# Kernel optimization log

Hardware: AMD Instinct MI355X
Metric: run time of the kernel (lower is better)

The kernel has to match this reference:

```python
import jax, jax.numpy as jnp
import numpy as np

B, N, D, R, NUM_HEADS, S = 8, 512, 256, 6, 3, 1000


def setup_inputs() -> dict:
    key = jax.random.key(0)
    ks = jax.random.split(key, 12)
    init = lambda k, shape: jax.random.normal(k, shape, jnp.float32) * 0.02
    return {
        "symbol_ids": jax.random.randint(ks[0], (B, N), 0, S),
        "positions": jax.random.normal(ks[1], (B, N, 2), jnp.float32),
        "sym_table": init(ks[2], (S, D)),
        "layer_table": init(ks[3], (S, D)),      # layer-0 interpretation embedding
        "rel_W": init(ks[4], (R, D, D)),          # per-relation Linear weights (in,out)
        "rel_b": init(ks[5], (R, D)),
        "h1_W": init(ks[6], (NUM_HEADS, D, D)),   # interpretation head Linear1
        "h1_b": init(ks[7], (NUM_HEADS, D)),
        "h2_W": init(ks[8], (NUM_HEADS, D)),      # interpretation head Linear2 (D->1)
        "h2_b": init(ks[9], (NUM_HEADS,)),
        "out_W": init(ks[10], (D, D)),
        "out_b": init(ks[11], (D,)),
    }


def _relation_type(dx, dy):
    # Vectorized version of PositionalGrammar._get_relation_type (if/elif chain)
    return jnp.select(
        [dy > 0.5, dy < -0.5, dx < -0.5, dx > 0.5,
         (jnp.abs(dx) < 0.3) & (jnp.abs(dy) < 0.3)],
        [0, 1, 2, 3, 4], 5)


def _positional_grammar(symbols, positions, rel_W, rel_b):
    # transformed[b,j] = symbols[b,j] + sum_{i!=j} (symbols[b,i] @ W_r(i,j) + b_r(i,j))
    dx = positions[:, None, :, 0] - positions[:, :, None, 0]  # [b,i,j]
    dy = positions[:, None, :, 1] - positions[:, :, None, 1]
    rel = _relation_type(dx, dy)                               # [b,i,j] int
    n = symbols.shape[1]
    not_self = ~jnp.eye(n, dtype=bool)
    # one-hot relation mask, self-pairs excluded: [b,i,j,r]
    M = ((rel[..., None] == jnp.arange(R)) & not_self[None, :, :, None]).astype(symbols.dtype)
    T = jnp.einsum('bid,rde->brie', symbols, rel_W)            # per-relation transform of sources
    contrib = jnp.einsum('bijr,brie->bje', M, T)               # scatter-add over sources i
    bias = jnp.einsum('bijr,re->bje', M, rel_b)                # per-pair bias accumulation
    return symbols + contrib + bias


def reference(symbol_ids, positions, sym_table, layer_table, rel_W, rel_b,
              h1_W, h1_b, h2_W, h2_b, out_W, out_b):
    # SymbolEmbedding (calendar_pos=None path; layer=0)
    symbols = sym_table[symbol_ids] + layer_table[symbol_ids]  # [B,N,D]
    # PositionalGrammar
    symbols = _positional_grammar(symbols, positions, rel_W, rel_b)
    # LayeredInterpretation: 3 heads of Linear-GELU-Linear(D->1)
    h = jax.nn.gelu(jnp.einsum('bnd,rde->brne', symbols, h1_W)
                    + h1_b[None, :, None, :], approximate=False)
    interp = jnp.einsum('brne,re->brn', h, h2_W) + h2_b[None, :, None]  # [B,3,N]
    # output projection
    output = symbols @ out_W + out_b
    return (output,
            interp[:, 0, :, None],   # exoteric  [B,N,1]
            interp[:, 1, :, None],   # esoteric
            interp[:, 2, :, None],   # sacred
            symbols)
```

## Files before the change

### kernel.cpp

```cpp
#include <hip/hip_runtime.h>
#include <hip/hip_bf16.h>
#include <math.h>

#define BB 8
#define NN 512
#define DD 256
#define BNT 4096

typedef __attribute__((ext_vector_type(8))) short short8;
typedef __attribute__((ext_vector_type(4))) float f32x4;

#define OFF_S0B   0u
#define OFF_TT    524288u
#define OFF_WCT   6815744u
#define OFF_WBT   7012352u
#define OFF_BB    7143424u
#define OFF_REL   7144448u

#define OUT0_OFF   0u
#define INTERP_OFF 1048576u
#define SYM_OFF    1060864u

__device__ __forceinline__ float gelu_exact(float x) {
    return 0.5f * x * (1.0f + erff(x * 0.70710678118654752f));
}

__device__ __forceinline__ ushort f2bf(float x) {
    __hip_bfloat16 h = __float2bfloat16(x);
    union { __hip_bfloat16 b; ushort u; } cv;
    cv.b = h;
    return cv.u;
}

__device__ __forceinline__ int rel_of(float dx, float dy) {
    int r = (fabsf(dx) < 0.3f && fabsf(dy) < 0.3f) ? 4 : 5;
    r = (dx >  0.5f) ? 3 : r;
    r = (dx < -0.5f) ? 2 : r;
    r = (dy < -0.5f) ? 1 : r;
    r = (dy >  0.5f) ? 0 : r;
    return r;
}

#define TILE_IDS()                                             \
    const int lane = tid & 63, w = tid >> 6;                   \
    const int wm = w >> 1, wn = w & 1;                         \
    const int quad = lane >> 4, l15 = lane & 15;               \
    const int sm = tid >> 2, sq = tid & 3;

#define MFMA_STEP(Abuf, Bbuf)                                                \
    {                                                                        \
        short8 af[2], bfr[2];                                                \
        _Pragma("unroll")                                                    \
        for (int mt = 0; mt < 2; mt++)                                       \
            af[mt] = *(const short8*)&(Abuf)[(quad * 64 + wm * 32 + mt * 16 + l15) * 8]; \
        _Pragma("unroll")                                                    \
        for (int nt = 0; nt < 2; nt++)                                       \
            bfr[nt] = *(const short8*)&(Bbuf)[(quad * 64 + wn * 32 + nt * 16 + l15) * 8]; \
        _Pragma("unroll")                                                    \
        for (int mt = 0; mt < 2; mt++)                                       \
            _Pragma("unroll")                                                \
            for (int nt = 0; nt < 2; nt++)                                   \
                acc[mt][nt] = __builtin_amdgcn_mfma_f32_16x16x32_bf16(       \
                    af[mt], bfr[nt], acc[mt][nt], 0, 0, 0);                  \
    }

#define ACC_INIT()                                             \
    f32x4 acc[2][2];                                           \
    _Pragma("unroll") for (int mt = 0; mt < 2; mt++)           \
    _Pragma("unroll") for (int nt = 0; nt < 2; nt++)           \
        acc[mt][nt] = (f32x4){0.f, 0.f, 0.f, 0.f};

#define FB_TILE  0
#define FB_OUTI  160
#define FB_BBIG  172
#define FB_GATH  173
#define FB_CLS   1197
#define FB_TOTAL 1709

__global__ __launch_bounds__(256) void front_kernel(
    const int* __restrict__ ids, const float* __restrict__ positions,
    const float* __restrict__ symt, const float* __restrict__ layt,
    const float* __restrict__ relW, const float* __restrict__ h1W,
    const float* __restrict__ outW, const float* __restrict__ h1b,
    const float* __restrict__ outb, const float* __restrict__ h2b,
    ushort* __restrict__ WcT, ushort* __restrict__ WbT,
    float* __restrict__ bbig, float* __restrict__ outI,
    float* __restrict__ symOut, ushort* __restrict__ s0b,
    unsigned char* __restrict__ rel)
{
    __shared__ float shbuf[64 * 65];
    int blk = blockIdx.x, tid = threadIdx.x;
    if (blk < FB_OUTI) {
        int kl = tid & 63, g4 = tid >> 6;
        const float* src; int srow, scol;
        ushort* dst; int drow, dstride, dcol;
        if (blk < 96) {
            int t = blk, rdt = t >> 2, et = t & 3;
            src = relW; srow = rdt * 64; scol = et * 64;
            dst = WcT; drow = et * 64; dstride = 1536; dcol = rdt * 64;
        } else if (blk < 144) {
            int t = blk - 96, r = t >> 4, dt = (t >> 2) & 3, et = t & 3;
            src = h1W + (size_t)r * DD * DD; srow = dt * 64; scol = et * 64;
            dst = WbT; drow = r * 256 + et * 64; dstride = 256; dcol = dt * 64;
        } else {
            int t = blk - 144, dt = t >> 2, et = t & 3;
            src = outW; srow = dt * 64; scol = et * 64;
            dst = WbT; drow = 768 + et * 64; dstride = 256; dcol = dt * 64;
        }
#pragma unroll
        for (int p = 0; p < 16; p++) {
            int rl = p * 4 + g4;
            shbuf[rl * 65 + kl] = src[(size_t)(srow + rl) * 256 + scol + kl];
        }
        __syncthreads();
#pragma unroll
        for (int q = 0; q < 16; q++) {
            int el = q * 4 + g4;
            dst[(size_t)(drow + el) * dstride + dcol + kl] = f2bf(shbuf[kl * 65 + el]);
        }
    } else if (blk < FB_BBIG) {
        int idx = (blk - FB_OUTI) * 256 + tid;
        float v = h2b[idx >> 10];
        ((float4*)outI)[idx] = (float4){v, v, v, v};
    } else if (blk < FB_GATH) {
        ((float4*)bbig)[tid] = (tid < 192) ? ((const float4*)h1b)[tid]
                                           : ((const float4*)outb)[tid - 192];
    } else if (blk < FB_CLS) {
        int row = (blk - FB_GATH) * 4 + (tid >> 6);
        int d = (tid & 63) * 4;
        int id = ids[row];
        float4 a = *(const float4*)&symt[(size_t)id * DD + d];
        float4 c = *(const float4*)&layt[(size_t)id * DD + d];
        float4 v = {a.x + c.x, a.y + c.y, a.z + c.z, a.w + c.w};
        *(float4*)&symOut[(size_t)row * DD + d] = v;
        union { ushort u[4]; uint2 q; } p;
        p.u[0] = f2bf(v.x); p.u[1] = f2bf(v.y); p.u[2] = f2bf(v.z); p.u[3] = f2bf(v.w);
        *(uint2*)&s0b[(size_t)row * DD + d] = p.q;
    } else {
        float* px = shbuf;
        float* py = shbuf + NN;
        int blk2 = blk - FB_CLS;
        int b = blk2 >> 6;
        int j0 = (blk2 & 63) << 3;
        int jl = tid >> 5, sub = tid & 31;
        for (int i = tid; i < NN; i += 256) {
            float2 p = ((const float2*)positions)[b * NN + i];
            px[i] = p.x; py[i] = p.y;
        }
        __syncthreads();
        int j = j0 + jl;
        float xj = px[j], yj = py[j];
        union { unsigned char u8[16]; uint4 v; } codes;
#pragma unroll
        for (int t = 0; t < 16; t++) {
            int i = sub * 16 + t;
            int r = rel_of(xj - px[i], yj - py[i]);
            r = (i == j) ? 6 : r;
            codes.u8[t] = (unsigned char)r;
        }
        *(uint4*)&rel[((size_t)(b * NN + j)) * NN + sub * 16] = codes.v;
    }
}

__global__ __launch_bounds__(256) void gemmT_kernel(
    const ushort* __restrict__ WcT, const ushort* __restrict__ s0b,
    const float* __restrict__ relb, ushort* __restrict__ TT)
{
    __shared__ ushort Als[2][2048], Bls[2][2048];
    int tid = threadIdx.x;
    int b = blockIdx.z;
    int rowM0 = blockIdx.y * 64;
    int col0 = blockIdx.x * 64;
    int r = rowM0 >> 8, e0 = rowM0 & 255;
    TILE_IDS();
    ACC_INIT();
    const ushort* gA = WcT + (size_t)(e0 + sm) * 1536 + r * 256 + sq * 8;
    const ushort* gB = s0b + ((size_t)(b * NN) + col0 + sm) * DD + sq * 8;
    const int lo = (sq * 64 + sm) * 8;

    *(uint4*)&Als[0][lo] = *(const uint4*)gA;
    *(uint4*)&Bls[0][lo] = *(const uint4*)gB;
#pragma unroll
    for (int i = 0; i < 8; i++) {
        __syncthreads();
        uint4 av2, bv2;
        if (i < 7) {
            av2 = *(const uint4*)(gA + (i + 1) * 32);
            bv2 = *(const uint4*)(gB + (i + 1) * 32);
        }
        MFMA_STEP(Als[i & 1], Bls[i & 1]);
        if (i < 7) {
            *(uint4*)&Als[(i + 1) & 1][lo] = av2;
            *(uint4*)&Bls[(i + 1) & 1][lo] = bv2;
        }
    }
#pragma unroll
    for (int mt = 0; mt < 2; mt++)
#pragma unroll
        for (int nt = 0; nt < 2; nt++)
#pragma unroll
            for (int v = 0; v < 4; v++) {
                int e = e0 + wm * 32 + mt * 16 + quad * 4 + v;
                int i = col0 + wn * 32 + nt * 16 + l15;
                TT[((size_t)(b * DD) + e) * 3072 + r * 512 + i] =
                    f2bf(acc[mt][nt][v] + relb[r * DD + e]);
            }
}

__global__ __launch_bounds__(256) void agg_gemm(
    const unsigned char* __restrict__ rel, const ushort* __restrict__ TT,
    float* __restrict__ symOut)
{
    __shared__ ushort Als[2][2048], Bls[2][2048];
    int tid = threadIdx.x;
    int z = blockIdx.z;
    int b = z / 3, rg = z - b * 3;
    int row0 = blockIdx.y * 64, col0 = blockIdx.x * 64;
    TILE_IDS();
    ACC_INIT();
    const unsigned char* gC = rel + ((size_t)(b * NN + row0 + sm)) * NN;
    const ushort* gB = TT + ((size_t)(b * DD) + col0 + sm) * 3072 + rg * 1024 + sq * 8;
    const int lo = (sq * 64 + sm) * 8;

#define AGG_LOADS(i, cw, bv)                                        \
    cw = *(const uint2*)(gC + (((i) * 32 + sq * 8) & 511));         \
    bv = *(const uint4*)(gB + (i) * 32);

#define AGG_STAGE(i, cw, bv, buf)                                   \
    {                                                               \
        int rr_ = 2 * rg + (((i) * 32) >> 9);                       \
        union alignas(16) { ushort u[8]; uint4 v; } am;             \
        _Pragma("unroll")                                           \
        for (int t = 0; t < 8; t++) {                               \
            unsigned int word = (t < 4) ? cw.x : cw.y;              \
            unsigned int code = (word >> (8 * (t & 3))) & 255u;     \
            am.u[t] = (code == (unsigned)rr_) ? 0x3F80 : 0;         \
        }                                                           \
        *(uint4*)&Als[buf][lo] = am.v;                              \
        *(uint4*)&Bls[buf][lo] = bv;                                \
    }

    uint2 cw0; uint4 bv0;
    AGG_LOADS(0, cw0, bv0);
    AGG_STAGE(0, cw0, bv0, 0);
    for (int i = 0; i < 32; i++) {
        __syncthreads();
        uint2 cw2 = cw0; uint4 bv2 = bv0;
        if (i < 31) { AGG_LOADS(i + 1, cw2, bv2); }
        MFMA_STEP(Als[i & 1], Bls[i & 1]);
        if (i < 31) { AGG_STAGE(i + 1, cw2, bv2, (i + 1) & 1); }
    }
#undef AGG_LOADS
#undef AGG_STAGE
#pragma unroll
    for (int mt = 0; mt < 2; mt++)
#pragma unroll
        for (int nt = 0; nt < 2; nt++)
#pragma unroll
            for (int v = 0; v < 4; v++) {
                int j = row0 + wm * 32 + mt * 16 + quad * 4 + v;
                int e = col0 + wn * 32 + nt * 16 + l15;
                atomicAdd(&symOut[((size_t)(b * NN) + j) * DD + e], acc[mt][nt][v]);
            }
}

__global__ __launch_bounds__(256) void gemm2_kernel(
    const float* __restrict__ symOut, const ushort* __restrict__ WbT,
    const float* __restrict__ bbig, const float* __restrict__ h2W,
    float* __restrict__ out0, float* __restrict__ outI)
{
    __shared__ ushort Als[2][2048], Bls[2][2048];
    int tid = threadIdx.x;
    int row0 = blockIdx.y * 64, col0 = blockIdx.x * 64;
    TILE_IDS();
    ACC_INIT();
    const float*  gA = symOut + (size_t)(row0 + sm) * DD + sq * 8;
    const ushort* gB = WbT    + (size_t)(col0 + sm) * DD + sq * 8;
    const int lo = (sq * 64 + sm) * 8;

#define G2_LOADS(i, a0, a1, bv)                                     \
    a0 = *(const float4*)(gA + (i) * 32);                           \
    a1 = *(const float4*)(gA + (i) * 32 + 4);                       \
    bv = *(const uint4*)(gB + (i) * 32);

#define G2_STAGE(a0, a1, bv, buf)                                   \
    {                                                               \
        union alignas(16) { ushort u[8]; uint4 v; } am;             \
        am.u[0] = f2bf(a0.x); am.u[1] = f2bf(a0.y);                 \
        am.u[2] = f2bf(a0.z); am.u[3] = f2bf(a0.w);                 \
        am.u[4] = f2bf(a1.x); am.u[5] = f2bf(a1.y);                 \
        am.u[6] = f2bf(a1.z); am.u[7] = f2bf(a1.w);                 \
        *(uint4*)&Als[buf][lo] = am.v;                              \
        *(uint4*)&Bls[buf][lo] = bv;                                \
    }

    float4 a0, a1; uint4 bv;
    G2_LOADS(0, a0, a1, bv);
    G2_STAGE(a0, a1, bv, 0);
#pragma unroll
    for (int i = 0; i < 8; i++) {
        __syncthreads();
        float4 a0n = a0, a1n = a1; uint4 bvn = bv;
        if (i < 7) { G2_LOADS(i + 1, a0n, a1n, bvn); }
        MFMA_STEP(Als[i & 1], Bls[i & 1]);
        if (i < 7) { G2_STAGE(a0n, a1n, bvn, (i + 1) & 1); }
    }
#undef G2_LOADS
#undef G2_STAGE
    if (col0 >= 768) {
#pragma unroll
        for (int nt = 0; nt < 2; nt++) {
            int c = col0 + wn * 32 + nt * 16 + l15;
            float bb = bbig[c];
#pragma unroll
            for (int mt = 0; mt < 2; mt++)
#pragma unroll
                for (int v = 0; v < 4; v++) {
                    int row = row0 + wm * 32 + mt * 16 + quad * 4 + v;
                    out0[(size_t)row * DD + (c - 768)] = acc[mt][nt][v] + bb;
                }
        }
    } else {
        int head = col0 >> 8;
        float part[2][4];
#pragma unroll
        for (int mt = 0; mt < 2; mt++)
#pragma unroll
            for (int v = 0; v < 4; v++) part[mt][v] = 0.f;
#pragma unroll
        for (int nt = 0; nt < 2; nt++) {
            int c = col0 + wn * 32 + nt * 16 + l15;
            float bb = bbig[c];
            float w2 = h2W[c];
#pragma unroll
            for (int mt = 0; mt < 2; mt++)
#pragma unroll
                for (int v = 0; v < 4; v++)
                    part[mt][v] += gelu_exact(acc[mt][nt][v] + bb) * w2;
        }
#pragma unroll
        for (int mt = 0; mt < 2; mt++)
#pragma unroll
            for (int v = 0; v < 4; v++) {
                float p = part[mt][v];
                p += __shfl_xor(p, 1); p += __shfl_xor(p, 2);
                p += __shfl_xor(p, 4); p += __shfl_xor(p, 8);
                if (l15 == 0) {
                    int row = row0 + wm * 32 + mt * 16 + quad * 4 + v;
                    atomicAdd(&outI[head * BNT + row], p);
                }
            }
    }
}

extern "C" void kernel_launch(void* const* d_in, const int* in_sizes, int n_in,
                              void* d_out, int out_size, void* d_ws, size_t ws_size,
                              hipStream_t stream)
{
    const int*   ids  = (const int*)d_in[0];
    const float* pos  = (const float*)d_in[1];
    const float* symt = (const float*)d_in[2];
    const float* layt = (const float*)d_in[3];
    const float* relW = (const float*)d_in[4];
    const float* relb = (const float*)d_in[5];
    const float* h1W  = (const float*)d_in[6];
    const float* h1b  = (const float*)d_in[7];
    const float* h2W  = (const float*)d_in[8];
    const float* h2b  = (const float*)d_in[9];
    const float* outW = (const float*)d_in[10];
    const float* outb = (const float*)d_in[11];
    float* out = (float*)d_out;
    float* ws  = (float*)d_ws;

    ushort* s0b  = (ushort*)(ws + OFF_S0B);
    ushort* TT   = (ushort*)(ws + OFF_TT);
    ushort* WcT  = (ushort*)(ws + OFF_WCT);
    ushort* WbT  = (ushort*)(ws + OFF_WBT);
    float*  bbig = ws + OFF_BB;
    unsigned char* rel = (unsigned char*)(ws + OFF_REL);

    front_kernel<<<FB_TOTAL, 256, 0, stream>>>(ids, pos, symt, layt, relW, h1W, outW,
                                               h1b, outb, h2b, WcT, WbT, bbig,
                                               out + INTERP_OFF, out + SYM_OFF, s0b, rel);
    gemmT_kernel<<<dim3(8, 24, 8), 256, 0, stream>>>(WcT, s0b, relb, TT);
    agg_gemm<<<dim3(4, 8, 24), 256, 0, stream>>>(rel, TT, out + SYM_OFF);
    gemm2_kernel<<<dim3(16, 64), 256, 0, stream>>>(out + SYM_OFF, WbT,
                                                   bbig, h2W,
                                                   out + OUT0_OFF, out + INTERP_OFF);
}
```

Before: 134.9 us.

## Widen GEMM tiles to 64x128 and split aggregation per relation

All three GEMM kernels now use 64x128 output tiles, with each wave computing 2x4 MFMA fragments instead of 2x2. This raises MFMA work per LDS A-fragment load and halves block counts along N. The aggregation kernel now assigns one relation per block (z = b*6 + r) over the 512-source K range with 16 steps, and builds the mask with a byte-XOR compare. That doubles the atomicAdd traffic into symOut but shortens each block's K loop. The larger tiles use more registers and LDS, which may reduce occupancy.

Measured after the change: 148.0 us. +9.7%, slower.

```diff
diff --git a/kernel.cpp b/kernel.cpp
--- a/kernel.cpp
+++ b/kernel.cpp
@@ -45,29 +45,30 @@
     const int lane = tid & 63, w = tid >> 6;                   \
     const int wm = w >> 1, wn = w & 1;                         \
     const int quad = lane >> 4, l15 = lane & 15;               \
-    const int sm = tid >> 2, sq = tid & 3;
-
-#define MFMA_STEP(Abuf, Bbuf)                                                \
+    const int sm = tid >> 2, sq = tid & 3;                     \
+    const int bc = tid & 127, bch = tid >> 7;
+
+#define MFMA_STEP24(Abuf, Bbuf)                                              \
     {                                                                        \
-        short8 af[2], bfr[2];                                                \
+        short8 af[2], bfr[4];                                                \
         _Pragma("unroll")                                                    \
         for (int mt = 0; mt < 2; mt++)                                       \
             af[mt] = *(const short8*)&(Abuf)[(quad * 64 + wm * 32 + mt * 16 + l15) * 8]; \
         _Pragma("unroll")                                                    \
-        for (int nt = 0; nt < 2; nt++)                                       \
-            bfr[nt] = *(const short8*)&(Bbuf)[(quad * 64 + wn * 32 + nt * 16 + l15) * 8]; \
+        for (int nt = 0; nt < 4; nt++)                                       \
+            bfr[nt] = *(const short8*)&(Bbuf)[(quad * 128 + wn * 64 + nt * 16 + l15) * 8]; \
         _Pragma("unroll")                                                    \
         for (int mt = 0; mt < 2; mt++)                                       \
             _Pragma("unroll")                                                \
-            for (int nt = 0; nt < 2; nt++)                                   \
+            for (int nt = 0; nt < 4; nt++)                                   \
                 acc[mt][nt] = __builtin_amdgcn_mfma_f32_16x16x32_bf16(       \
                     af[mt], bfr[nt], acc[mt][nt], 0, 0, 0);                  \
     }
 
-#define ACC_INIT()                                             \
-    f32x4 acc[2][2];                                           \
+#define ACC_INIT24()                                           \
+    f32x4 acc[2][4];                                           \
     _Pragma("unroll") for (int mt = 0; mt < 2; mt++)           \
-    _Pragma("unroll") for (int nt = 0; nt < 2; nt++)           \
+    _Pragma("unroll") for (int nt = 0; nt < 4; nt++)           \
         acc[mt][nt] = (f32x4){0.f, 0.f, 0.f, 0.f};
 
 #define FB_TILE  0
@@ -166,42 +167,48 @@
     const ushort* __restrict__ WcT, const ushort* __restrict__ s0b,
     const float* __restrict__ relb, ushort* __restrict__ TT)
 {
-    __shared__ ushort Als[2][2048], Bls[2][2048];
+    __shared__ ushort Als[2][2048], Bls[2][4096];
     int tid = threadIdx.x;
     int b = blockIdx.z;
     int rowM0 = blockIdx.y * 64;
-    int col0 = blockIdx.x * 64;
+    int col0 = blockIdx.x * 128;
     int r = rowM0 >> 8, e0 = rowM0 & 255;
     TILE_IDS();
-    ACC_INIT();
-    const ushort* gA = WcT + (size_t)(e0 + sm) * 1536 + r * 256 + sq * 8;
-    const ushort* gB = s0b + ((size_t)(b * NN) + col0 + sm) * DD + sq * 8;
-    const int lo = (sq * 64 + sm) * 8;
-
-    *(uint4*)&Als[0][lo] = *(const uint4*)gA;
-    *(uint4*)&Bls[0][lo] = *(const uint4*)gB;
+    ACC_INIT24();
+    const ushort* gA  = WcT + (size_t)(e0 + sm) * 1536 + r * 256 + sq * 8;
+    const ushort* gB0 = s0b + ((size_t)(b * NN) + col0 + bc) * DD + bch * 8;
+    const ushort* gB1 = gB0 + 16;
+    const int loA  = (sq * 64 + sm) * 8;
+    const int loB0 = (bch * 128 + bc) * 8;
+    const int loB1 = ((bch + 2) * 128 + bc) * 8;
+
+    *(uint4*)&Als[0][loA]  = *(const uint4*)gA;
+    *(uint4*)&Bls[0][loB0] = *(const uint4*)gB0;
+    *(uint4*)&Bls[0][loB1] = *(const uint4*)gB1;
 #pragma unroll
     for (int i = 0; i < 8; i++) {
         __syncthreads();
-        uint4 av2, bv2;
+        uint4 av, bv0, bv1;
         if (i < 7) {
-            av2 = *(const uint4*)(gA + (i + 1) * 32);
-            bv2 = *(const uint4*)(gB + (i + 1) * 32);
-        }
-        MFMA_STEP(Als[i & 1], Bls[i & 1]);
+            av  = *(const uint4*)(gA  + (i + 1) * 32);
+            bv0 = *(const uint4*)(gB0 + (i + 1) * 32);
+            bv1 = *(const uint4*)(gB1 + (i + 1) * 32);
+        }
+        MFMA_STEP24(Als[i & 1], Bls[i & 1]);
         if (i < 7) {
-            *(uint4*)&Als[(i + 1) & 1][lo] = av2;
-            *(uint4*)&Bls[(i + 1) & 1][lo] = bv2;
+            *(uint4*)&Als[(i + 1) & 1][loA]  = av;
+            *(uint4*)&Bls[(i + 1) & 1][loB0] = bv0;
+            *(uint4*)&Bls[(i + 1) & 1][loB1] = bv1;
         }
     }
 #pragma unroll
     for (int mt = 0; mt < 2; mt++)
 #pragma unroll
-        for (int nt = 0; nt < 2; nt++)
+        for (int nt = 0; nt < 4; nt++)
 #pragma unroll
             for (int v = 0; v < 4; v++) {
                 int e = e0 + wm * 32 + mt * 16 + quad * 4 + v;
-                int i = col0 + wn * 32 + nt * 16 + l15;
+                int i = col0 + wn * 64 + nt * 16 + l15;
                 TT[((size_t)(b * DD) + e) * 3072 + r * 512 + i] =
                     f2bf(acc[mt][nt][v] + relb[r * DD + e]);
             }
@@ -211,55 +218,62 @@
     const unsigned char* __restrict__ rel, const ushort* __restrict__ TT,
     float* __restrict__ symOut)
 {
-    __shared__ ushort Als[2][2048], Bls[2][2048];
+    __shared__ ushort Als[2][2048], Bls[2][4096];
     int tid = threadIdx.x;
     int z = blockIdx.z;
-    int b = z / 3, rg = z - b * 3;
-    int row0 = blockIdx.y * 64, col0 = blockIdx.x * 64;
+    int b = z / 6;
+    unsigned rr = (unsigned)(z - b * 6);
+    int row0 = blockIdx.y * 64, col0 = blockIdx.x * 128;
     TILE_IDS();
-    ACC_INIT();
-    const unsigned char* gC = rel + ((size_t)(b * NN + row0 + sm)) * NN;
-    const ushort* gB = TT + ((size_t)(b * DD) + col0 + sm) * 3072 + rg * 1024 + sq * 8;
-    const int lo = (sq * 64 + sm) * 8;
-
-#define AGG_LOADS(i, cw, bv)                                        \
-    cw = *(const uint2*)(gC + (((i) * 32 + sq * 8) & 511));         \
-    bv = *(const uint4*)(gB + (i) * 32);
-
-#define AGG_STAGE(i, cw, bv, buf)                                   \
+    ACC_INIT24();
+    const unsigned char* gC = rel + ((size_t)(b * NN + row0 + sm)) * NN + sq * 8;
+    const ushort* gB0 = TT + ((size_t)(b * DD) + col0 + bc) * 3072 + rr * 512 + bch * 8;
+    const ushort* gB1 = gB0 + 16;
+    const int loA  = (sq * 64 + sm) * 8;
+    const int loB0 = (bch * 128 + bc) * 8;
+    const int loB1 = ((bch + 2) * 128 + bc) * 8;
+
+#define AGG_STAGE(cw, bv0, bv1, buf)                                \
     {                                                               \
-        int rr_ = 2 * rg + (((i) * 32) >> 9);                       \
+        unsigned m_ = rr * 0x01010101u;                             \
+        unsigned x_ = cw.x ^ m_, y_ = cw.y ^ m_;                    \
         union alignas(16) { ushort u[8]; uint4 v; } am;             \
         _Pragma("unroll")                                           \
-        for (int t = 0; t < 8; t++) {                               \
-            unsigned int word = (t < 4) ? cw.x : cw.y;              \
-            unsigned int code = (word >> (8 * (t & 3))) & 255u;     \
-            am.u[t] = (code == (unsigned)rr_) ? 0x3F80 : 0;         \
+        for (int t = 0; t < 4; t++) {                               \
+            am.u[t]     = (((x_ >> (8 * t)) & 255u) == 0u) ? 0x3F80 : 0; \
+            am.u[t + 4] = (((y_ >> (8 * t)) & 255u) == 0u) ? 0x3F80 : 0; \
         }                                                           \
-        *(uint4*)&Als[buf][lo] = am.v;                              \
-        *(uint4*)&Bls[buf][lo] = bv;                                \
-    }
-
-    uint2 cw0; uint4 bv0;
-    AGG_LOADS(0, cw0, bv0);
-    AGG_STAGE(0, cw0, bv0, 0);
-    for (int i = 0; i < 32; i++) {
+        *(uint4*)&Als[buf][loA]  = am.v;                            \
+        *(uint4*)&Bls[buf][loB0] = bv0;                             \
+        *(uint4*)&Bls[buf][loB1] = bv1;                             \
+    }
+
+    uint2 cw0 = *(const uint2*)gC;
+    uint4 bv0 = *(const uint4*)gB0;
+    uint4 bv1 = *(const uint4*)gB1;
+    AGG_STAGE(cw0, bv0, bv1, 0);
+#pragma unroll
+    for (int i = 0; i < 16; i++) {
         __syncthreads();
-        uint2 cw2 = cw0; uint4 bv2 = bv0;
-        if (i < 31) { AGG_LOADS(i + 1, cw2, bv2); }
-        MFMA_STEP(Als[i & 1], Bls[i & 1]);
-        if (i < 31) { AGG_STAGE(i + 1, cw2, bv2, (i + 1) & 1); }
-    }
-#undef AGG_LOADS
+        uint2 cwn = cw0; uint4 bvn0 = bv0, bvn1 = bv1;
+        if (i < 15) {
+            cwn  = *(const uint2*)(gC  + (i + 1) * 32);
+            bvn0 = *(const uint4*)(gB0 + (i + 1) * 32);
+            bvn1 = *(const uint4*)(gB1 + (i + 1) * 32);
+        }
+        MFMA_STEP24(Als[i & 1], Bls[i & 1]);
+        if (i < 15) { AGG_STAGE(cwn, bvn0, bvn1, (i + 1) & 1); }
+        cw0 = cwn; bv0 = bvn0; bv1 = bvn1;
+    }
 #undef AGG_STAGE
 #pragma unroll
     for (int mt = 0; mt < 2; mt++)
 #pragma unroll
-        for (int nt = 0; nt < 2; nt++)
+        for (int nt = 0; nt < 4; nt++)
 #pragma unroll
             for (int v = 0; v < 4; v++) {
                 int j = row0 + wm * 32 + mt * 16 + quad * 4 + v;
-                int e = col0 + wn * 32 + nt * 16 + l15;
+                int e = col0 + wn * 64 + nt * 16 + l15;
                 atomicAdd(&symOut[((size_t)(b * NN) + j) * DD + e], acc[mt][nt][v]);
             }
 }
@@ -269,48 +283,54 @@
     const float* __restrict__ bbig, const float* __restrict__ h2W,
     float* __restrict__ out0, float* __restrict__ outI)
 {
-    __shared__ ushort Als[2][2048], Bls[2][2048];
+    __shared__ ushort Als[2][2048], Bls[2][4096];
     int tid = threadIdx.x;
-    int row0 = blockIdx.y * 64, col0 = blockIdx.x * 64;
+    int row0 = blockIdx.y * 64, col0 = blockIdx.x * 128;
     TILE_IDS();
-    ACC_INIT();
-    const float*  gA = symOut + (size_t)(row0 + sm) * DD + sq * 8;
-    const ushort* gB = WbT    + (size_t)(col0 + sm) * DD + sq * 8;
-    const int lo = (sq * 64 + sm) * 8;
-
-#define G2_LOADS(i, a0, a1, bv)                                     \
-    a0 = *(const float4*)(gA + (i) * 32);                           \
-    a1 = *(const float4*)(gA + (i) * 32 + 4);                       \
-    bv = *(const uint4*)(gB + (i) * 32);
-
-#define G2_STAGE(a0, a1, bv, buf)                                   \
+    ACC_INIT24();
+    const float*  gA  = symOut + (size_t)(row0 + sm) * DD + sq * 8;
+    const ushort* gB0 = WbT    + (size_t)(col0 + bc) * DD + bch * 8;
+    const ushort* gB1 = gB0 + 16;
+    const int loA  = (sq * 64 + sm) * 8;
+    const int loB0 = (bch * 128 + bc) * 8;
+    const int loB1 = ((bch + 2) * 128 + bc) * 8;
+
+#define G2_STAGE(a0, a1, bv0, bv1, buf)                             \
     {                                                               \
         union alignas(16) { ushort u[8]; uint4 v; } am;             \
         am.u[0] = f2bf(a0.x); am.u[1] = f2bf(a0.y);                 \
         am.u[2] = f2bf(a0.z); am.u[3] = f2bf(a0.w);                 \
         am.u[4] = f2bf(a1.x); am.u[5] = f2bf(a1.y);                 \
         am.u[6] = f2bf(a1.z); am.u[7] = f2bf(a1.w);                 \
-        *(uint4*)&Als[buf][lo] = am.v;                              \
-        *(uint4*)&Bls[buf][lo] = bv;                                \
-    }
-
-    float4 a0, a1; uint4 bv;
-    G2_LOADS(0, a0, a1, bv);
-    G2_STAGE(a0, a1, bv, 0);
+        *(uint4*)&Als[buf][loA]  = am.v;                            \
+        *(uint4*)&Bls[buf][loB0] = bv0;                             \
+        *(uint4*)&Bls[buf][loB1] = bv1;                             \
+    }
+
+    float4 a0 = *(const float4*)gA;
+    float4 a1 = *(const float4*)(gA + 4);
+    uint4 bv0 = *(const uint4*)gB0;
+    uint4 bv1 = *(const uint4*)gB1;
+    G2_STAGE(a0, a1, bv0, bv1, 0);
 #pragma unroll
     for (int i = 0; i < 8; i++) {
         __syncthreads();
-        float4 a0n = a0, a1n = a1; uint4 bvn = bv;
-        if (i < 7) { G2_LOADS(i + 1, a0n, a1n, bvn); }
-        MFMA_STEP(Als[i & 1], Bls[i & 1]);
-        if (i < 7) { G2_STAGE(a0n, a1n, bvn, (i + 1) & 1); }
-    }
-#undef G2_LOADS
+        float4 a0n = a0, a1n = a1; uint4 bvn0 = bv0, bvn1 = bv1;
+        if (i < 7) {
+            a0n  = *(const float4*)(gA + (i + 1) * 32);
+            a1n  = *(const float4*)(gA + (i + 1) * 32 + 4);
+            bvn0 = *(const uint4*)(gB0 + (i + 1) * 32);
+            bvn1 = *(const uint4*)(gB1 + (i + 1) * 32);
+        }
+        MFMA_STEP24(Als[i & 1], Bls[i & 1]);
+        if (i < 7) { G2_STAGE(a0n, a1n, bvn0, bvn1, (i + 1) & 1); }
+        a0 = a0n; a1 = a1n; bv0 = bvn0; bv1 = bvn1;
+    }
 #undef G2_STAGE
     if (col0 >= 768) {
 #pragma unroll
-        for (int nt = 0; nt < 2; nt++) {
-            int c = col0 + wn * 32 + nt * 16 + l15;
+        for (int nt = 0; nt < 4; nt++) {
+            int c = col0 + wn * 64 + nt * 16 + l15;
             float bb = bbig[c];
 #pragma unroll
             for (int mt = 0; mt < 2; mt++)
@@ -328,8 +348,8 @@
 #pragma unroll
             for (int v = 0; v < 4; v++) part[mt][v] = 0.f;
 #pragma unroll
-        for (int nt = 0; nt < 2; nt++) {
-            int c = col0 + wn * 32 + nt * 16 + l15;
+        for (int nt = 0; nt < 4; nt++) {
+            int c = col0 + wn * 64 + nt * 16 + l15;
             float bb = bbig[c];
             float w2 = h2W[c];
 #pragma unroll
@@ -382,9 +402,9 @@
     front_kernel<<<FB_TOTAL, 256, 0, stream>>>(ids, pos, symt, layt, relW, h1W, outW,
                                                h1b, outb, h2b, WcT, WbT, bbig,
                                                out + INTERP_OFF, out + SYM_OFF, s0b, rel);
-    gemmT_kernel<<<dim3(8, 24, 8), 256, 0, stream>>>(WcT, s0b, relb, TT);
-    agg_gemm<<<dim3(4, 8, 24), 256, 0, stream>>>(rel, TT, out + SYM_OFF);
-    gemm2_kernel<<<dim3(16, 64), 256, 0, stream>>>(out + SYM_OFF, WbT,
-                                                   bbig, h2W,
-                                                   out + OUT0_OFF, out + INTERP_OFF);
-}
+    gemmT_kernel<<<dim3(4, 24, 8), 256, 0, stream>>>(WcT, s0b, relb, TT);
+    agg_gemm<<<dim3(2, 8, 48), 256, 0, stream>>>(rel, TT, out + SYM_OFF);
+    gemm2_kernel<<<dim3(8, 64), 256, 0, stream>>>(out + SYM_OFF, WbT,
+                                                  bbig, h2W,
+                                                  out + OUT0_OFF, out + INTERP_OFF);
+}
```
